# Optimization experiments

Hardware: AMD Instinct MI355X
Metric: run time of the kernel (lower is better)

The kernel has to match this reference:

```python
import jax, jax.numpy as jnp
import numpy as np

N_HEADS = 16
N_DIM = 1024
H_DIM = N_DIM // N_HEADS


def setup_inputs() -> dict:
    key = jax.random.key(0)
    ks = jax.random.split(key, 9)
    s = 1.0 / np.sqrt(N_DIM)
    x = jax.random.normal(ks[0], (4, 2048, N_DIM), dtype=jnp.float32)
    Wq = jax.random.uniform(ks[1], (N_DIM, N_DIM), jnp.float32, -s, s)
    bq = jax.random.uniform(ks[2], (N_DIM,), jnp.float32, -s, s)
    Wk = jax.random.uniform(ks[3], (N_DIM, N_DIM), jnp.float32, -s, s)
    bk = jax.random.uniform(ks[4], (N_DIM,), jnp.float32, -s, s)
    Wv = jax.random.uniform(ks[5], (N_DIM, N_DIM), jnp.float32, -s, s)
    bv = jax.random.uniform(ks[6], (N_DIM,), jnp.float32, -s, s)
    Wp = jax.random.uniform(ks[7], (N_DIM, N_DIM), jnp.float32, -s, s)
    bp = jax.random.uniform(ks[8], (N_DIM,), jnp.float32, -s, s)
    return {"x": x, "Wq": Wq, "bq": bq, "Wk": Wk, "bk": bk,
            "Wv": Wv, "bv": bv, "Wp": Wp, "bp": bp}


def _split_heads(y):
    # [b, t, (nh*hd)] -> [nh, b, t, hd]
    b, t, _ = y.shape
    return y.reshape(b, t, N_HEADS, H_DIM).transpose(2, 0, 1, 3)


def reference(x, Wq, bq, Wk, bk, Wv, bv, Wp, bp):
    q = _split_heads(x @ Wq.T + bq)
    k = _split_heads(x @ Wk.T + bk)
    v = _split_heads(x @ Wv.T + bv)
    # NOTE: original module applies NO 1/sqrt(d) scaling
    energies = jnp.einsum('hbqd,hbkd->hbqk', q, k)
    attn = jax.nn.softmax(energies, axis=-1)  # dropout disabled (eval)
    out = jnp.einsum('hbqk,hbkd->hbqd', attn, v)
    # [nh, b, t, hd] -> [b, t, nh*hd]
    b, t = out.shape[1], out.shape[2]
    out = out.transpose(1, 2, 0, 3).reshape(b, t, N_DIM)
    return out @ Wp.T + bp
```

## Files before the change

### kernel.cpp

```cpp
#include <hip/hip_runtime.h>
#include <hip/hip_bf16.h>


typedef short short8 __attribute__((ext_vector_type(8)));
typedef float float4v __attribute__((ext_vector_type(4)));

#define MFMA16(a, b, c) __builtin_amdgcn_mfma_f32_16x16x32_bf16((a), (b), (c), 0, 0, 0)
#define LOG2E 1.4426950408889634f

#define B_SZ 4
#define T_SZ 2048
#define D_SZ 1024
#define NH 16
#define HD 64
#define M_SZ (B_SZ * T_SZ)
#define MW_SZ (D_SZ * D_SZ)

__device__ __forceinline__ unsigned short f2bf(float f) {
  unsigned int u = __float_as_uint(f);
  u += 0x7fffu + ((u >> 16) & 1u);
  return (unsigned short)(u >> 16);
}

__device__ __forceinline__ float fexp2(float x) {
#if __has_builtin(__builtin_amdgcn_exp2f)
  return __builtin_amdgcn_exp2f(x);
#else
  return exp2f(x);
#endif
}

__device__ __forceinline__ void gl_lds16(const unsigned short* g, unsigned short* l) {
  __builtin_amdgcn_global_load_lds(
      (const __attribute__((address_space(1))) unsigned int*)g,
      (__attribute__((address_space(3))) unsigned int*)l, 16, 0, 0);
}

__global__ __launch_bounds__(256) void cvt_all(const float* __restrict__ x,
                                               const float* __restrict__ w0,
                                               const float* __restrict__ w1,
                                               const float* __restrict__ w2,
                                               const float* __restrict__ w3,
                                               const float* __restrict__ b0,
                                               const float* __restrict__ b1,
                                               const float* __restrict__ b2,
                                               unsigned short* __restrict__ xb,
                                               unsigned short* __restrict__ wout,
                                               float* __restrict__ bout) {
  const long blk = blockIdx.x;
  if (blk < 8192) {
    long i = (blk * 256 + threadIdx.x) * 4;
    float4 v = *(const float4*)(x + i);
    uint2 o;
    o.x = (unsigned)f2bf(v.x) | ((unsigned)f2bf(v.y) << 16);
    o.y = (unsigned)f2bf(v.z) | ((unsigned)f2bf(v.w) << 16);
    *(uint2*)(xb + i) = o;
  } else if (blk < 12288) {
    long i = ((blk - 8192) * 256 + threadIdx.x) * 4;
    int which = (int)(i >> 20);
    const float* src = which == 0 ? w0 : which == 1 ? w1 : which == 2 ? w2 : w3;
    float scale = which == 0 ? LOG2E : 1.0f;
    long j = i - (long)which * MW_SZ;
    float4 v = *(const float4*)(src + j);
    uint2 o;
    o.x = (unsigned)f2bf(v.x * scale) | ((unsigned)f2bf(v.y * scale) << 16);
    o.y = (unsigned)f2bf(v.z * scale) | ((unsigned)f2bf(v.w * scale) << 16);
    *(uint2*)(wout + i) = o;
  } else {
    int i = (int)((blk - 12288) * 256 + threadIdx.x) * 4;
    float4 v;
    if (i < 1024) {
      v = *(const float4*)(b0 + i);
      v.x *= LOG2E; v.y *= LOG2E; v.z *= LOG2E; v.w *= LOG2E;
    } else if (i < 2048) {
      v = *(const float4*)(b1 + (i - 1024));
    } else {
      v = *(const float4*)(b2 + (i - 2048));
    }
    *(float4*)(bout + i) = v;
  }
}

__global__ __launch_bounds__(256, 3) void gemm_qkv(const unsigned short* __restrict__ A,
                                                   const unsigned short* __restrict__ W,
                                                   const float* __restrict__ bias,
                                                   unsigned short* __restrict__ Qb,
                                                   unsigned short* __restrict__ Kb,
                                                   unsigned short* __restrict__ Vt) {
  __shared__ __align__(16) unsigned short smem[17408];
  unsigned short* As = smem;
  unsigned short* Bs = smem + 8192;
  unsigned short* Ct = smem;
  const int tid = threadIdx.x;
  const int wave = tid >> 6, lane = tid & 63;
  const int q = lane >> 4, ln = lane & 15;
  const int wm = (wave >> 1) * 64, wn = (wave & 1) * 64;
  const long m0 = (long)blockIdx.y * 128;
  const long n0 = (long)blockIdx.x * 128;
  const int srow = lane >> 3, scol = (lane & 7) * 8;
  const int K = D_SZ;

  float4v acc[4][4] = {};

  for (int k0 = 0; k0 < K; k0 += 64) {
    for (int t = 0; t < 4; ++t) {
      int seg = wave * 4 + t;
      int row = seg * 8 + srow;
      gl_lds16(A + (m0 + row) * (long)K + k0 + scol, As + seg * 512);
      gl_lds16(W + (n0 + row) * (long)K + k0 + scol, Bs + seg * 512);
    }
    __syncthreads();
    for (int ks = 0; ks < 2; ++ks) {
      short8 af[4], bf[4];
      for (int i = 0; i < 4; ++i)
        af[i] = *(const short8*)(As + (wm + i * 16 + ln) * 64 + ks * 32 + q * 8);
      for (int j = 0; j < 4; ++j)
        bf[j] = *(const short8*)(Bs + (wn + j * 16 + ln) * 64 + ks * 32 + q * 8);
      for (int i = 0; i < 4; ++i)
        for (int j = 0; j < 4; ++j)
          acc[i][j] = MFMA16(af[i], bf[j], acc[i][j]);
    }
    __syncthreads();
  }

  if ((int)n0 < 2048) {
    unsigned short* dst = (int)n0 < 1024 ? Qb : Kb;
    int coff = (int)n0 < 1024 ? 0 : 1024;
    for (int i = 0; i < 4; ++i) {
      long rowb = m0 + wm + i * 16 + q * 4;
      for (int j = 0; j < 4; ++j) {
        long col = n0 + wn + j * 16 + ln;
        float bv = bias[col];
        for (int r = 0; r < 4; ++r)
          dst[(rowb + r) * (long)D_SZ + col - coff] = f2bf(acc[i][j][r] + bv);
      }
    }
  } else {
    for (int i = 0; i < 4; ++i)
      for (int j = 0; j < 4; ++j) {
        int col_l = wn + j * 16 + ln;
        float bv = bias[n0 + col_l];
        __hip_bfloat162 lo =
            __float22bfloat162_rn(make_float2(acc[i][j][0] + bv, acc[i][j][1] + bv));
        __hip_bfloat162 hi =
            __float22bfloat162_rn(make_float2(acc[i][j][2] + bv, acc[i][j][3] + bv));
        uint2 w;
        w.x = *(unsigned*)&lo;
        w.y = *(unsigned*)&hi;
        *(uint2*)(Ct + col_l * 136 + wm + i * 16 + q * 4) = w;
      }
    __syncthreads();
    for (int it = 0; it < 8; ++it) {
      int idx = tid + it * 256;
      int c = idx >> 4, rb = idx & 15;
      uint4 v = *(const uint4*)(Ct + c * 136 + rb * 8);
      *(uint4*)(Vt + (n0 - 2048 + c) * (long)M_SZ + m0 + rb * 8) = v;
    }
  }
}

__global__ __launch_bounds__(256, 3) void gemm_proj(const unsigned short* __restrict__ A,
                                                    const unsigned short* __restrict__ W,
                                                    const float* __restrict__ bias,
                                                    float* __restrict__ Cf) {
  __shared__ __align__(16) unsigned short As[128 * 64];
  __shared__ __align__(16) unsigned short Bs[128 * 64];
  const int tid = threadIdx.x;
  const int wave = tid >> 6, lane = tid & 63;
  const int q = lane >> 4, ln = lane & 15;
  const int wm = (wave >> 1) * 64, wn = (wave & 1) * 64;
  const long m0 = (long)blockIdx.y * 128;
  const long n0 = (long)blockIdx.x * 128;
  const int srow = lane >> 3, scol = (lane & 7) * 8;
  const int K = D_SZ;

  float4v acc[4][4] = {};
  for (int k0 = 0; k0 < K; k0 += 64) {
    for (int t = 0; t < 4; ++t) {
      int seg = wave * 4 + t;
      int row = seg * 8 + srow;
      gl_lds16(A + (m0 + row) * (long)K + k0 + scol, As + seg * 512);
      gl_lds16(W + (n0 + row) * (long)K + k0 + scol, Bs + seg * 512);
    }
    __syncthreads();
    for (int ks = 0; ks < 2; ++ks) {
      short8 af[4], bf[4];
      for (int i = 0; i < 4; ++i)
        af[i] = *(const short8*)(As + (wm + i * 16 + ln) * 64 + ks * 32 + q * 8);
      for (int j = 0; j < 4; ++j)
        bf[j] = *(const short8*)(Bs + (wn + j * 16 + ln) * 64 + ks * 32 + q * 8);
      for (int i = 0; i < 4; ++i)
        for (int j = 0; j < 4; ++j)
          acc[i][j] = MFMA16(af[i], bf[j], acc[i][j]);
    }
    __syncthreads();
  }
  for (int i = 0; i < 4; ++i) {
    long rowb = m0 + wm + i * 16 + q * 4;
    for (int j = 0; j < 4; ++j) {
      long col = n0 + wn + j * 16 + ln;
      float bv = bias[col];
      for (int r = 0; r < 4; ++r)
        Cf[(rowb + r) * (long)D_SZ + col] = acc[i][j][r] + bv;
    }
  }
}

__global__ __launch_bounds__(512, 4) void attn_kernel(const unsigned short* __restrict__ Qb,
                                                      const unsigned short* __restrict__ Kb,
                                                      const unsigned short* __restrict__ Vt,
                                                      unsigned short* __restrict__ Ob) {
  __shared__ __align__(16) unsigned short KV[16384];
  __shared__ __align__(16) unsigned short Pp[5120];

  const int tid = threadIdx.x;
  const int wave = tid >> 6, lane = tid & 63;
  const int q = lane >> 4, ln = lane & 15;
  const int l7 = lane & 7, l3 = lane >> 3;
  const int qt = blockIdx.x, h = blockIdx.y, b = blockIdx.z;

  const long baseQ = ((long)b * T_SZ + qt * 128) * D_SZ + h * HD;
  const long baseK = (long)b * T_SZ * D_SZ + h * HD;
  const long baseV = (long)h * HD * M_SZ + (long)b * T_SZ;
  const int cs = ((l7 ^ l3) * 8);

  short8 qf[2];
  for (int ks = 0; ks < 2; ++ks)
    qf[ks] = *(const short8*)(Qb + baseQ + (long)(wave * 16 + ln) * D_SZ + ks * 32 + q * 8);

  float4v o[4] = {};
  float lp = 0.f;
  unsigned short* Ppw = Pp + wave * (16 * 40);
  const int swz = (ln & 7) * 8;

#define STAGE(kt_, base_)                                                                \
  {                                                                                      \
    int row = wave * 8 + l3;                                                             \
    gl_lds16(Kb + baseK + (long)((kt_)*64 + row) * D_SZ + cs, (base_) + wave * 512);     \
    gl_lds16(Vt + baseV + (long)row * M_SZ + (kt_)*64 + cs, (base_) + 4096 + wave * 512);\
  }

  STAGE(0, KV)

  for (int kt = 0; kt < 32; ++kt) {
    unsigned short* cur = KV + (kt & 1) * 8192;
    unsigned short* nxt = KV + ((kt & 1) ^ 1) * 8192;
    __syncthreads();
    if (kt < 31) { STAGE(kt + 1, nxt) }

    short8 kf[4][2];
    for (int c = 0; c < 4; ++c)
      for (int ks = 0; ks < 2; ++ks)
        kf[c][ks] = *(const short8*)(cur + (c * 16 + ln) * 64 + ((ks * 32 + q * 8) ^ swz));
    float4v s[4];
    __builtin_amdgcn_s_setprio(1);
    for (int c = 0; c < 4; ++c) {
      float4v z = {};
      z = MFMA16(kf[c][0], qf[0], z);
      z = MFMA16(kf[c][1], qf[1], z);
      s[c] = z;
    }
    __builtin_amdgcn_s_setprio(0);

    for (int ks = 0; ks < 2; ++ks) {
      for (int cl = 0; cl < 2; ++cl) {
        int c = 2 * ks + cl;
        float p0 = fexp2(s[c][0]);
        float p1 = fexp2(s[c][1]);
        float p2 = fexp2(s[c][2]);
        float p3 = fexp2(s[c][3]);
        lp += (p0 + p1) + (p2 + p3);
        __hip_bfloat162 lo = __float22bfloat162_rn(make_float2(p0, p1));
        __hip_bfloat162 hi = __float22bfloat162_rn(make_float2(p2, p3));
        uint2 w;
        w.x = *(unsigned*)&lo;
        w.y = *(unsigned*)&hi;
        *(uint2*)(Ppw + ln * 40 + cl * 16 + q * 4) = w;
      }
      short8 vf[4];
      for (int j = 0; j < 4; ++j)
        vf[j] = *(const short8*)(cur + 4096 + (j * 16 + ln) * 64 + ((ks * 32 + q * 8) ^ swz));
      short8 pf = *(const short8*)(Ppw + ln * 40 + q * 8);
      __builtin_amdgcn_s_setprio(1);
      for (int j = 0; j < 4; ++j)
        o[j] = MFMA16(pf, vf[j], o[j]);
      __builtin_amdgcn_s_setprio(0);
    }
  }

  {
    float l = lp;
    l += __shfl_xor(l, 16, 64);
    l += __shfl_xor(l, 32, 64);
    float inv = 1.f / l;
    for (int r = 0; r < 4; ++r) {
      int src = (lane & 48) | (q * 4 + r);
      float invr = __shfl(inv, src, 64);
      int row = qt * 128 + wave * 16 + q * 4 + r;
      long base = ((long)b * T_SZ + row) * D_SZ + h * HD;
      for (int j = 0; j < 4; ++j)
        Ob[base + j * 16 + ln] = f2bf(o[j][r] * invr);
    }
  }
#undef STAGE
}

extern "C" void kernel_launch(void* const* d_in, const int* in_sizes, int n_in,
                              void* d_out, int out_size, void* d_ws, size_t ws_size,
                              hipStream_t stream) {
  const float* x = (const float*)d_in[0];
  const float* Wq = (const float*)d_in[1];
  const float* bq = (const float*)d_in[2];
  const float* Wk = (const float*)d_in[3];
  const float* bk = (const float*)d_in[4];
  const float* Wv = (const float*)d_in[5];
  const float* bv = (const float*)d_in[6];
  const float* Wp = (const float*)d_in[7];
  const float* bp = (const float*)d_in[8];
  float* out = (float*)d_out;

  const long MX = (long)M_SZ * D_SZ;
  const long MW = (long)MW_SZ;
  unsigned short* ws = (unsigned short*)d_ws;
  unsigned short* xb = ws;
  unsigned short* Wcat = xb + MX;
  float* bcat = (float*)(Wcat + 4 * MW);
  unsigned short* Qb = (unsigned short*)(bcat + 3072);
  unsigned short* Kb = Qb + MX;
  unsigned short* Vtb = Kb + MX;
  unsigned short* Ob = Vtb + MX;

  cvt_all<<<12291, 256, 0, stream>>>(x, Wq, Wk, Wv, Wp, bq, bk, bv, xb, Wcat, bcat);

  dim3 gq(3072 / 128, M_SZ / 128);
  gemm_qkv<<<gq, 256, 0, stream>>>(xb, Wcat, bcat, Qb, Kb, Vtb);

  dim3 ag(T_SZ / 128, NH, B_SZ);
  attn_kernel<<<ag, 512, 0, stream>>>(Qb, Kb, Vtb, Ob);

  dim3 gp(D_SZ / 128, M_SZ / 128);
  gemm_proj<<<gp, 256, 0, stream>>>(Ob, Wcat + 3 * MW, bp, out);
}
```

Measured before the change: 282.7 us.

## Double query rows per wave in attention to reuse K/V tiles

Each wave in the attention kernel now handles 32 query rows (two 16-row MFMA tiles) instead of 16, so each block covers 256 queries and the grid halves to 512 blocks. The K and V tiles staged in LDS are reused across twice as many queries, which halves K/V global traffic and the number of staging barriers per query. The grid is also flattened with head and batch in the low bits, which changes block scheduling order. The s_setprio hints were removed. In exchange, register pressure roughly doubles for the accumulators and score tiles, occupancy may drop, and 512 blocks may underfill the 256 CUs.

```diff
diff --git a/kernel.cpp b/kernel.cpp
--- a/kernel.cpp
+++ b/kernel.cpp
@@ -211,26 +211,31 @@
                                                       const unsigned short* __restrict__ Vt,
                                                       unsigned short* __restrict__ Ob) {
   __shared__ __align__(16) unsigned short KV[16384];
-  __shared__ __align__(16) unsigned short Pp[5120];
+  __shared__ __align__(16) unsigned short Pp[10240];
 
   const int tid = threadIdx.x;
   const int wave = tid >> 6, lane = tid & 63;
   const int q = lane >> 4, ln = lane & 15;
   const int l7 = lane & 7, l3 = lane >> 3;
-  const int qt = blockIdx.x, h = blockIdx.y, b = blockIdx.z;
-
-  const long baseQ = ((long)b * T_SZ + qt * 128) * D_SZ + h * HD;
+  const int bid = blockIdx.x;
+  const int qt = bid >> 6;
+  const int hb = bid & 63;
+  const int h = hb & 15, b = hb >> 4;
+
+  const long baseQ = ((long)b * T_SZ + qt * 256) * D_SZ + h * HD;
   const long baseK = (long)b * T_SZ * D_SZ + h * HD;
   const long baseV = (long)h * HD * M_SZ + (long)b * T_SZ;
   const int cs = ((l7 ^ l3) * 8);
 
-  short8 qf[2];
-  for (int ks = 0; ks < 2; ++ks)
-    qf[ks] = *(const short8*)(Qb + baseQ + (long)(wave * 16 + ln) * D_SZ + ks * 32 + q * 8);
-
-  float4v o[4] = {};
-  float lp = 0.f;
-  unsigned short* Ppw = Pp + wave * (16 * 40);
+  short8 qf[2][2];
+  for (int i = 0; i < 2; ++i)
+    for (int ks = 0; ks < 2; ++ks)
+      qf[i][ks] = *(const short8*)(Qb + baseQ + (long)(wave * 32 + i * 16 + ln) * D_SZ +
+                                   ks * 32 + q * 8);
+
+  float4v o[2][4] = {};
+  float lp[2] = {};
+  unsigned short* Ppw = Pp + wave * (32 * 40);
   const int swz = (ln & 7) * 8;
 
 #define STAGE(kt_, base_)                                                                \
@@ -252,54 +257,55 @@
     for (int c = 0; c < 4; ++c)
       for (int ks = 0; ks < 2; ++ks)
         kf[c][ks] = *(const short8*)(cur + (c * 16 + ln) * 64 + ((ks * 32 + q * 8) ^ swz));
-    float4v s[4];
-    __builtin_amdgcn_s_setprio(1);
-    for (int c = 0; c < 4; ++c) {
-      float4v z = {};
-      z = MFMA16(kf[c][0], qf[0], z);
-      z = MFMA16(kf[c][1], qf[1], z);
-      s[c] = z;
-    }
-    __builtin_amdgcn_s_setprio(0);
+    float4v s[4][2];
+    for (int c = 0; c < 4; ++c)
+      for (int i = 0; i < 2; ++i) {
+        float4v z = {};
+        z = MFMA16(kf[c][0], qf[i][0], z);
+        z = MFMA16(kf[c][1], qf[i][1], z);
+        s[c][i] = z;
+      }
 
     for (int ks = 0; ks < 2; ++ks) {
-      for (int cl = 0; cl < 2; ++cl) {
-        int c = 2 * ks + cl;
-        float p0 = fexp2(s[c][0]);
-        float p1 = fexp2(s[c][1]);
-        float p2 = fexp2(s[c][2]);
-        float p3 = fexp2(s[c][3]);
-        lp += (p0 + p1) + (p2 + p3);
-        __hip_bfloat162 lo = __float22bfloat162_rn(make_float2(p0, p1));
-        __hip_bfloat162 hi = __float22bfloat162_rn(make_float2(p2, p3));
-        uint2 w;
-        w.x = *(unsigned*)&lo;
-        w.y = *(unsigned*)&hi;
-        *(uint2*)(Ppw + ln * 40 + cl * 16 + q * 4) = w;
-      }
+      for (int i = 0; i < 2; ++i)
+        for (int cl = 0; cl < 2; ++cl) {
+          int c = 2 * ks + cl;
+          float p0 = fexp2(s[c][i][0]);
+          float p1 = fexp2(s[c][i][1]);
+          float p2 = fexp2(s[c][i][2]);
+          float p3 = fexp2(s[c][i][3]);
+          lp[i] += (p0 + p1) + (p2 + p3);
+          __hip_bfloat162 lo = __float22bfloat162_rn(make_float2(p0, p1));
+          __hip_bfloat162 hi = __float22bfloat162_rn(make_float2(p2, p3));
+          uint2 w;
+          w.x = *(unsigned*)&lo;
+          w.y = *(unsigned*)&hi;
+          *(uint2*)(Ppw + (i * 16 + ln) * 40 + cl * 16 + q * 4) = w;
+        }
       short8 vf[4];
       for (int j = 0; j < 4; ++j)
         vf[j] = *(const short8*)(cur + 4096 + (j * 16 + ln) * 64 + ((ks * 32 + q * 8) ^ swz));
-      short8 pf = *(const short8*)(Ppw + ln * 40 + q * 8);
-      __builtin_amdgcn_s_setprio(1);
-      for (int j = 0; j < 4; ++j)
-        o[j] = MFMA16(pf, vf[j], o[j]);
-      __builtin_amdgcn_s_setprio(0);
-    }
-  }
-
-  {
-    float l = lp;
+      short8 pf[2];
+      for (int i = 0; i < 2; ++i)
+        pf[i] = *(const short8*)(Ppw + (i * 16 + ln) * 40 + q * 8);
+      for (int i = 0; i < 2; ++i)
+        for (int j = 0; j < 4; ++j)
+          o[i][j] = MFMA16(pf[i], vf[j], o[i][j]);
+    }
+  }
+
+  for (int i = 0; i < 2; ++i) {
+    float l = lp[i];
     l += __shfl_xor(l, 16, 64);
     l += __shfl_xor(l, 32, 64);
     float inv = 1.f / l;
     for (int r = 0; r < 4; ++r) {
       int src = (lane & 48) | (q * 4 + r);
       float invr = __shfl(inv, src, 64);
-      int row = qt * 128 + wave * 16 + q * 4 + r;
+      int row = qt * 256 + wave * 32 + i * 16 + q * 4 + r;
       long base = ((long)b * T_SZ + row) * D_SZ + h * HD;
       for (int j = 0; j < 4; ++j)
-        Ob[base + j * 16 + ln] = f2bf(o[j][r] * invr);
+        Ob[base + j * 16 + ln] = f2bf(o[i][j][r] * invr);
     }
   }
 #undef STAGE
@@ -335,8 +341,7 @@
   dim3 gq(3072 / 128, M_SZ / 128);
   gemm_qkv<<<gq, 256, 0, stream>>>(xb, Wcat, bcat, Qb, Kb, Vtb);
 
-  dim3 ag(T_SZ / 128, NH, B_SZ);
-  attn_kernel<<<ag, 512, 0, stream>>>(Qb, Kb, Vtb, Ob);
+  attn_kernel<<<512, 512, 0, stream>>>(Qb, Kb, Vtb, Ob);
 
   dim3 gp(D_SZ / 128, M_SZ / 128);
   gemm_proj<<<gp, 256, 0, stream>>>(Ob, Wcat + 3 * MW, bp, out);
```

Result: faster. 270.3 us (-4.4%).
